# Performance work log

Hardware: AMD Instinct MI355X
Metric: run time of the kernel (lower is better)

Reference implementation:

```python
import jax, jax.numpy as jnp
from jax import lax
import numpy as np

H = 512      # hidden_size
NF = 64      # nfeatures
NL = 2       # num_layers
OUT = 1      # output_size
B, T = 64, 512


def _uniform(key, shape, scale):
    return jax.random.uniform(key, shape, jnp.float32, -scale, scale)


def setup_inputs() -> dict:
    key = jax.random.key(0)
    ks = jax.random.split(key, 12)
    s = 1.0 / np.sqrt(H)  # PyTorch LSTM/Linear init scale
    return {
        "x": jax.random.normal(ks[0], (B, T, NF), jnp.float32),
        # layer 0 (input NF -> H), PyTorch gate order i,f,g,o along 4H axis
        "W_ih0": _uniform(ks[1], (4 * H, NF), s),
        "W_hh0": _uniform(ks[2], (4 * H, H), s),
        "b_ih0": _uniform(ks[3], (4 * H,), s),
        "b_hh0": _uniform(ks[4], (4 * H,), s),
        # layer 1 (input H -> H)
        "W_ih1": _uniform(ks[5], (4 * H, H), s),
        "W_hh1": _uniform(ks[6], (4 * H, H), s),
        "b_ih1": _uniform(ks[7], (4 * H,), s),
        "b_hh1": _uniform(ks[8], (4 * H,), s),
        # final linear head
        "W_fc": _uniform(ks[9], (OUT, H), s),
        "b_fc": _uniform(ks[10], (OUT,), s),
    }


def _lstm_layer(x, W_ih, W_hh, b_ih, b_hh):
    """x: [B, T, D_in] -> hidden sequence [B, T, H]. Zero initial state."""
    b, t, _ = x.shape
    h0 = jnp.zeros((b, H), x.dtype)
    c0 = jnp.zeros((b, H), x.dtype)
    # precompute input projections for all timesteps: [T, B, 4H]
    xp = jnp.swapaxes(jnp.einsum('btd,gd->btg', x, W_ih) + b_ih + b_hh, 0, 1)

    def step(carry, xt):
        h, c = carry
        gates = xt + h @ W_hh.T  # [B, 4H]
        i, f, g, o = jnp.split(gates, 4, axis=-1)
        i = jax.nn.sigmoid(i)
        f = jax.nn.sigmoid(f)
        g = jnp.tanh(g)
        o = jax.nn.sigmoid(o)
        c = f * c + i * g
        h = o * jnp.tanh(c)
        return (h, c), h

    _, hs = lax.scan(step, (h0, c0), xp)  # hs: [T, B, H]
    return jnp.swapaxes(hs, 0, 1)


def reference(x, W_ih0, W_hh0, b_ih0, b_hh0, W_ih1, W_hh1, b_ih1, b_hh1, W_fc, b_fc):
    h = _lstm_layer(x, W_ih0, W_hh0, b_ih0, b_hh0)
    h = _lstm_layer(h, W_ih1, W_hh1, b_ih1, b_hh1)
    return h @ W_fc.T + b_fc  # [B, T, OUT]
```

## Files before the change

kernel.cpp:

```cpp
#include <hip/hip_runtime.h>

#define T_STEPS 512
#define BATCH   64
#define HID     512

typedef __attribute__((ext_vector_type(8))) short short8;
typedef __attribute__((ext_vector_type(4))) float f32x4;

__device__ __forceinline__ unsigned short f2bf(float f){
  unsigned u = __float_as_uint(f);
  u += 0x7FFF + ((u >> 16) & 1);
  return (unsigned short)(u >> 16);
}
__device__ __forceinline__ float bf2f(unsigned short s){
  return __uint_as_float(((unsigned)s) << 16);
}
__device__ __forceinline__ f32x4 mfma16(short8 a, short8 b, f32x4 c){
  return __builtin_amdgcn_mfma_f32_16x16x32_bf16(a, b, c, 0, 0, 0);
}
__device__ __forceinline__ float sigf(float x){
  return 1.0f / (1.0f + exp2f(-1.44269504f * x));
}
__device__ __forceinline__ float tanh_(float x){
  float e = exp2f(2.88539008f * x);
  return 1.0f - 2.0f / (1.0f + e);
}


__device__ __forceinline__ void pollL0(const int* flags0, int target){
  if (threadIdx.x < 64){
    int lane = threadIdx.x;
    int guard = 0;
    for (;;){
      int v = (lane < 32)
        ? __hip_atomic_load(&flags0[lane*32], __ATOMIC_RELAXED, __HIP_MEMORY_SCOPE_AGENT)
        : target;
      if (__ballot(v >= target) == ~0ull) break;
      __builtin_amdgcn_s_sleep(1);
      if (++guard > (1 << 20)) break;
    }
  }
  __builtin_amdgcn_fence(__ATOMIC_ACQUIRE, "workgroup");
  asm volatile("" ::: "memory");
  __syncthreads();
}

__device__ __forceinline__ void pollL1(const int* flags0, const int* flags1, int t){
  if (threadIdx.x < 64){
    int lane = threadIdx.x;
    const int* p = (lane < 32) ? &flags0[lane*32] : &flags1[(lane-32)*32];
    int tgt = (lane < 32) ? t + 1 : t;
    int guard = 0;
    for (;;){
      int v = __hip_atomic_load(p, __ATOMIC_RELAXED, __HIP_MEMORY_SCOPE_AGENT);
      if (__ballot(v >= tgt) == ~0ull) break;
      __builtin_amdgcn_s_sleep(1);
      if (++guard > (1 << 20)) break;
    }
  }
  __builtin_amdgcn_fence(__ATOMIC_ACQUIRE, "workgroup");
  asm volatile("" ::: "memory");
  __syncthreads();
}

__device__ __forceinline__ void signalSlot(int* slot, int val){
  __builtin_amdgcn_fence(__ATOMIC_RELEASE, "workgroup");
  asm volatile("" ::: "memory");
  __hip_atomic_store(slot, val, __ATOMIC_RELAXED, __HIP_MEMORY_SCOPE_AGENT);
}

template<int NKB>
__device__ __forceinline__ void loadB(const unsigned short* __restrict__ Wg, int K, int kstart,
                                      int l15, int l4, short8 B[4][NKB]){
  #pragma unroll
  for (int tt = 0; tt < 4; ++tt)
    #pragma unroll
    for (int kb = 0; kb < NKB; ++kb)
      B[tt][kb] = *(const short8*)(Wg + (long)(tt*16 + l15)*K + kstart + kb*32 + l4*8);
}

template<int NKB>
__device__ __forceinline__ void gemmA(const unsigned short* __restrict__ Ab, long rs,
                                      int l15, int l4, const short8 B[4][NKB], f32x4 acc[4][4]){
  #pragma unroll
  for (int kb = 0; kb < NKB; ++kb){
    short8 a[4];
    #pragma unroll
    for (int m = 0; m < 4; ++m)
      a[m] = *(const short8*)(Ab + (long)(m*16 + l15)*rs + kb*32 + l4*8);
    #pragma unroll
    for (int m = 0; m < 4; ++m)
      #pragma unroll
      for (int tt = 0; tt < 4; ++tt)
        acc[m][tt] = mfma16(B[tt][kb], a[m], acc[m][tt]);
  }
}

__device__ __forceinline__ void reduceWrite(float* red, int w, int l15, int l4, f32x4 acc[4][4]){
  #pragma unroll
  for (int m = 0; m < 4; ++m){
    if (m == w) continue;
    int mi = (m > w) ? m - 1 : m;
    #pragma unroll
    for (int tt = 0; tt < 4; ++tt){
      float* p = red + (w*12 + mi*4 + tt)*320 + l15*20 + l4*4;
      *(f32x4*)p = acc[m][tt];
    }
  }
}
__device__ __forceinline__ void reduceRead(const float* red, int w, int l15, int l4,
                                           f32x4 gf[4], f32x4 acc[4][4]){
  #pragma unroll
  for (int tt = 0; tt < 4; ++tt) gf[tt] = acc[w][tt];
  #pragma unroll
  for (int v = 0; v < 4; ++v){
    if (v == w) continue;
    int mi = (w > v) ? w - 1 : w;
    #pragma unroll
    for (int tt = 0; tt < 4; ++tt){
      const float* p = red + (v*12 + mi*4 + tt)*320 + l15*20 + l4*4;
      gf[tt] += *(const f32x4*)p;
    }
  }
}

__device__ __forceinline__ void gatesStore(f32x4 gf[4], f32x4& cst,
                                           unsigned short* __restrict__ hdst){
  f32x4 hh;
  #pragma unroll
  for (int r = 0; r < 4; ++r){
    float iv = sigf(gf[0][r]), fv = sigf(gf[1][r]);
    float gv = tanh_(gf[2][r]), ov = sigf(gf[3][r]);
    float cv = fv * cst[r] + iv * gv;
    cst[r] = cv;
    hh[r] = ov * tanh_(cv);
  }
  unsigned long long pk = (unsigned long long)f2bf(hh[0])
    | ((unsigned long long)f2bf(hh[1]) << 16)
    | ((unsigned long long)f2bf(hh[2]) << 32)
    | ((unsigned long long)f2bf(hh[3]) << 48);
  __hip_atomic_store((unsigned long long*)hdst, pk, __ATOMIC_RELAXED, __HIP_MEMORY_SCOPE_AGENT);
}

template<int NXB, int NHB>
__device__ void l0_loop(int g, int w, int lane,
                        const unsigned short* __restrict__ Wg,
                        const float* __restrict__ bias0,
                        const unsigned short* __restrict__ xb,
                        unsigned short* __restrict__ h0seq,
                        int* flags0, float* red, int hk0){
  int l15 = lane & 15, l4 = lane >> 4;
  short8 Bx[4][(NXB > 0) ? NXB : 1];
  if constexpr (NXB > 0) loadB<NXB>(Wg, 576, 0, l15, l4, Bx);
  short8 Bh[4][NHB];
  loadB<NHB>(Wg, 576, 64 + hk0, l15, l4, Bh);
  f32x4 bsv[4];
  #pragma unroll
  for (int tt = 0; tt < 4; ++tt) bsv[tt] = *(const f32x4*)&bias0[(g*4 + tt)*16 + l4*4];
  f32x4 cst = {0.f, 0.f, 0.f, 0.f};
  int b = w*16 + l15, colb = g*16 + l4*4;

  for (int t = 0; t < T_STEPS; ++t){
    f32x4 acc[4][4];
    #pragma unroll
    for (int m = 0; m < 4; ++m)
      #pragma unroll
      for (int tt = 0; tt < 4; ++tt) acc[m][tt] = (f32x4){0.f,0.f,0.f,0.f};
    if constexpr (NXB > 0)
      gemmA<NXB>(xb + (long)t*64, (long)T_STEPS*64, l15, l4, Bx, acc);
    if (t) pollL0(flags0, t);
    if (t)
      gemmA<NHB>(h0seq + (long)(t-1)*BATCH*HID + hk0, HID, l15, l4, Bh, acc);
    reduceWrite(red, w, l15, l4, acc);
    __syncthreads();
    f32x4 gf[4];
    reduceRead(red, w, l15, l4, gf, acc);
    #pragma unroll
    for (int tt = 0; tt < 4; ++tt) gf[tt] += bsv[tt];
    gatesStore(gf, cst, h0seq + (long)t*BATCH*HID + (long)b*HID + colb);
    __syncthreads();
    if (threadIdx.x == 0) signalSlot(&flags0[g*32], t + 1);
  }
}

__device__ void l1_loop(int g, int w, int lane,
                        const unsigned short* __restrict__ Wg,
                        const float* __restrict__ bias1,
                        const unsigned short* __restrict__ h0seq,
                        unsigned short* __restrict__ h1seq,
                        int* flags0, int* flags1, float* red){
  int l15 = lane & 15, l4 = lane >> 4;
  short8 Bh[4][8];
  loadB<8>(Wg, 1024, w*256, l15, l4, Bh);
  f32x4 bsv[4];
  #pragma unroll
  for (int tt = 0; tt < 4; ++tt) bsv[tt] = *(const f32x4*)&bias1[(g*4 + tt)*16 + l4*4];
  f32x4 cst = {0.f, 0.f, 0.f, 0.f};
  int b = w*16 + l15, colb = g*16 + l4*4;

  for (int t = 0; t < T_STEPS; ++t){
    pollL1(flags0, flags1, t);
    f32x4 acc[4][4];
    #pragma unroll
    for (int m = 0; m < 4; ++m)
      #pragma unroll
      for (int tt = 0; tt < 4; ++tt) acc[m][tt] = (f32x4){0.f,0.f,0.f,0.f};
    if (w < 2)
      gemmA<8>(h0seq + (long)t*BATCH*HID + w*256, HID, l15, l4, Bh, acc);
    else if (t)
      gemmA<8>(h1seq + (long)(t-1)*BATCH*HID + (w-2)*256, HID, l15, l4, Bh, acc);
    reduceWrite(red, w, l15, l4, acc);
    __syncthreads();
    f32x4 gf[4];
    reduceRead(red, w, l15, l4, gf, acc);
    #pragma unroll
    for (int tt = 0; tt < 4; ++tt) gf[tt] += bsv[tt];
    gatesStore(gf, cst, h1seq + (long)t*BATCH*HID + (long)b*HID + colb);
    __syncthreads();
    if (threadIdx.x == 0) signalSlot(&flags1[g*32], t + 1);
  }
}

extern "C" __global__ void __launch_bounds__(256, 1)
lstm_persist(const unsigned short* __restrict__ Wpk0,
             const unsigned short* __restrict__ Wpk1,
             const float* __restrict__ bias0, const float* __restrict__ bias1,
             const unsigned short* __restrict__ xb,
             unsigned short* __restrict__ h0seq, unsigned short* __restrict__ h1seq,
             int* flags0, int* flags1){
  __shared__ float red[15360];
  int wg = blockIdx.x;
  int role = wg >> 5;
  int g = wg & 31;
  int w = threadIdx.x >> 6;
  int lane = threadIdx.x & 63;

  if (role == 0){
    const unsigned short* Wg = Wpk0 + (long)g*4*16*576;
    switch (w){
      case 0:  l0_loop<2,3>(g, 0, lane, Wg, bias0, xb, h0seq, flags0, red, 0);   break;
      case 1:  l0_loop<0,5>(g, 1, lane, Wg, bias0, xb, h0seq, flags0, red, 96);  break;
      case 2:  l0_loop<0,4>(g, 2, lane, Wg, bias0, xb, h0seq, flags0, red, 256); break;
      default: l0_loop<0,4>(g, 3, lane, Wg, bias0, xb, h0seq, flags0, red, 384); break;
    }
  } else {
    const unsigned short* Wg = Wpk1 + (long)g*4*16*1024;
    l1_loop(g, w, lane, Wg, bias1, h0seq, h1seq, flags0, flags1, red);
  }
}

extern "C" __global__ void prep_kernel(const float* __restrict__ x,
    const float* __restrict__ Wih0, const float* __restrict__ Whh0,
    const float* __restrict__ bih0, const float* __restrict__ bhh0,
    const float* __restrict__ Wih1, const float* __restrict__ Whh1,
    const float* __restrict__ bih1, const float* __restrict__ bhh1,
    unsigned short* __restrict__ Wpk0, unsigned short* __restrict__ Wpk1,
    float* __restrict__ bias0, float* __restrict__ bias1,
    unsigned short* __restrict__ xb, int* __restrict__ syncm){
  long gid = (long)blockIdx.x * blockDim.x + threadIdx.x;
  long gs  = (long)gridDim.x * blockDim.x;
  const long NW0 = 32L*4*16*576;
  const long NW1 = 32L*4*16*1024;
  const long NX  = 64L*512*64;

  for (long i = gid; i < NW0; i += gs){
    int k = (int)(i % 576);
    long q = i / 576;
    int r  = (int)(q & 15);
    long q2 = q >> 4;
    int tt = (int)(q2 & 3);
    int g  = (int)(q2 >> 2);
    int row = tt*512 + g*16 + r;
    float v = (k < 64) ? Wih0[(long)row*64 + k] : Whh0[(long)row*512 + (k - 64)];
    Wpk0[i] = f2bf(v);
  }
  for (long i = gid; i < NW1; i += gs){
    int k = (int)(i & 1023);
    long q = i >> 10;
    int r  = (int)(q & 15);
    long q2 = q >> 4;
    int tt = (int)(q2 & 3);
    int g  = (int)(q2 >> 2);
    int row = tt*512 + g*16 + r;
    float v = (k < 512) ? Wih1[(long)row*512 + k] : Whh1[(long)row*512 + (k - 512)];
    Wpk1[i] = f2bf(v);
  }
  for (long i = gid; i < 2048; i += gs){
    int r = (int)(i & 15);
    int tt = (int)((i >> 4) & 3);
    int g  = (int)(i >> 6);
    int row = tt*512 + g*16 + r;
    bias0[i] = bih0[row] + bhh0[row];
    bias1[i] = bih1[row] + bhh1[row];
  }
  for (long i = gid; i < NX; i += gs) xb[i] = f2bf(x[i]);
  for (long i = gid; i < 2048; i += gs) syncm[i] = 0;
}

extern "C" __global__ void head_kernel(const unsigned short* __restrict__ h1seq,
    const float* __restrict__ wfc, const float* __restrict__ bfc,
    float* __restrict__ out){
  int t = blockIdx.x;
  int tid = threadIdx.x;
  int b = tid >> 2, q = tid & 3;
  const unsigned short* hp = h1seq + ((long)t*BATCH + b)*HID + q*128;
  const float* wp = wfc + q*128;
  float s = 0.f;
  #pragma unroll
  for (int i = 0; i < 16; ++i){
    short8 v = *(const short8*)(hp + i*8);
    #pragma unroll
    for (int e = 0; e < 8; ++e)
      s += bf2f((unsigned short)v[e]) * wp[i*8 + e];
  }
  s += __shfl_xor(s, 1, 64);
  s += __shfl_xor(s, 2, 64);
  if (q == 0) out[(long)b*T_STEPS + t] = s + bfc[0];
}

extern "C" void kernel_launch(void* const* d_in, const int* in_sizes, int n_in,
                              void* d_out, int out_size, void* d_ws, size_t ws_size,
                              hipStream_t stream){
  const float* x    = (const float*)d_in[0];
  const float* Wih0 = (const float*)d_in[1];
  const float* Whh0 = (const float*)d_in[2];
  const float* bih0 = (const float*)d_in[3];
  const float* bhh0 = (const float*)d_in[4];
  const float* Wih1 = (const float*)d_in[5];
  const float* Whh1 = (const float*)d_in[6];
  const float* bih1 = (const float*)d_in[7];
  const float* bhh1 = (const float*)d_in[8];
  const float* wfc  = (const float*)d_in[9];
  const float* bfc  = (const float*)d_in[10];
  float* out = (float*)d_out;

  char* p = (char*)d_ws;
  auto carve = [&](size_t bytes) -> void* {
    void* r = (void*)p;
    p += (bytes + 255) & ~(size_t)255;
    return r;
  };
  unsigned short* Wpk0  = (unsigned short*)carve(32L*4*16*576*2);
  unsigned short* Wpk1  = (unsigned short*)carve(32L*4*16*1024*2);
  float* bias0 = (float*)carve(2048*4);
  float* bias1 = (float*)carve(2048*4);
  unsigned short* xb    = (unsigned short*)carve(64L*512*64*2);
  unsigned short* h0seq = (unsigned short*)carve(512L*64*512*2);
  unsigned short* h1seq = (unsigned short*)carve(512L*64*512*2);
  int* syncm   = (int*)carve(8192);
  int* flags0 = syncm;
  int* flags1 = syncm + 1024;

  hipLaunchKernelGGL(prep_kernel, dim3(1024), dim3(256), 0, stream,
                     x, Wih0, Whh0, bih0, bhh0, Wih1, Whh1, bih1, bhh1,
                     Wpk0, Wpk1, bias0, bias1, xb, syncm);
  hipLaunchKernelGGL(lstm_persist, dim3(64), dim3(256), 0, stream,
                     Wpk0, Wpk1, bias0, bias1, xb, h0seq, h1seq, flags0, flags1);
  hipLaunchKernelGGL(head_kernel, dim3(512), dim3(256), 0, stream,
                     h1seq, wfc, bfc, out);
}
```

Measured before the change: 5.261 ms.

## Co-locate persistent LSTM blocks on one XCD and use L2-scoped flag sync

Launches 512 blocks but keeps only every eighth one, so that under round-robin dispatch all 64 working blocks land on the same XCD. At startup the blocks check whether they can all see each other's flags through L2-coherent (sc0) loads. If they agree, they use sc0 loads and stores for the step flags and plain stores for the h outputs, instead of agent-scope atomics, and the spin loops drop `s_sleep`. The goal is lower cross-block handoff latency on each of the 512 serial timesteps. The cost is that the working blocks share fewer CUs, and correctness depends on the dispatch placement and on the verdict check; there is a fallback to the original atomic path.

Result: slower. 8.966 ms (+70.4%).

```diff
diff --git a/kernel.cpp b/kernel.cpp
--- a/kernel.cpp
+++ b/kernel.cpp
@@ -26,47 +26,56 @@
   return 1.0f - 2.0f / (1.0f + e);
 }
 
-
-__device__ __forceinline__ void pollL0(const int* flags0, int target){
-  if (threadIdx.x < 64){
-    int lane = threadIdx.x;
-    int guard = 0;
-    for (;;){
-      int v = (lane < 32)
-        ? __hip_atomic_load(&flags0[lane*32], __ATOMIC_RELAXED, __HIP_MEMORY_SCOPE_AGENT)
-        : target;
-      if (__ballot(v >= target) == ~0ull) break;
-      __builtin_amdgcn_s_sleep(1);
-      if (++guard > (1 << 20)) break;
-    }
-  }
+__device__ __forceinline__ int fload(const int* p){
+  int v;
+  asm volatile("global_load_dword %0, %1, off sc0\n\ts_waitcnt vmcnt(0)"
+               : "=&v"(v) : "v"(p) : "memory");
+  return v;
+}
+__device__ __forceinline__ void fstore(int* p, int v){
+  asm volatile("global_store_dword %0, %1, off sc0" :: "v"(p), "v"(v) : "memory");
+}
+__device__ __forceinline__ int aload(const int* p){
+  return __hip_atomic_load(p, __ATOMIC_RELAXED, __HIP_MEMORY_SCOPE_AGENT);
+}
+__device__ __forceinline__ void astore(int* p, int v){
+  __hip_atomic_store(p, v, __ATOMIC_RELAXED, __HIP_MEMORY_SCOPE_AGENT);
+}
+
+template<bool FAST>
+__device__ __forceinline__ void spin0(int* fF, int* fS, int target){
+  int lane = threadIdx.x & 63;
+  int idx = (lane & 31)*32;
+  int guard = 0;
+  for (;;){
+    int v = FAST ? fload(fF + idx) : aload(fS + idx);
+    if (__ballot(v >= target) == ~0ull) break;
+    if (++guard > (1 << 16)) break;
+  }
+  asm volatile("" ::: "memory");
   __builtin_amdgcn_fence(__ATOMIC_ACQUIRE, "workgroup");
+}
+template<bool FAST>
+__device__ __forceinline__ void spin1(int* f0F, int* f0S, int* f1F, int* f1S, int t){
+  int lane = threadIdx.x & 63;
+  int idx = (lane & 31)*32;
+  int tgt = (lane < 32) ? t + 1 : t;
+  int* pF = (lane < 32) ? f0F + idx : f1F + idx;
+  int* pS = (lane < 32) ? f0S + idx : f1S + idx;
+  int guard = 0;
+  for (;;){
+    int v = FAST ? fload(pF) : aload(pS);
+    if (__ballot(v >= tgt) == ~0ull) break;
+    if (++guard > (1 << 16)) break;
+  }
   asm volatile("" ::: "memory");
-  __syncthreads();
-}
-
-__device__ __forceinline__ void pollL1(const int* flags0, const int* flags1, int t){
-  if (threadIdx.x < 64){
-    int lane = threadIdx.x;
-    const int* p = (lane < 32) ? &flags0[lane*32] : &flags1[(lane-32)*32];
-    int tgt = (lane < 32) ? t + 1 : t;
-    int guard = 0;
-    for (;;){
-      int v = __hip_atomic_load(p, __ATOMIC_RELAXED, __HIP_MEMORY_SCOPE_AGENT);
-      if (__ballot(v >= tgt) == ~0ull) break;
-      __builtin_amdgcn_s_sleep(1);
-      if (++guard > (1 << 20)) break;
-    }
-  }
   __builtin_amdgcn_fence(__ATOMIC_ACQUIRE, "workgroup");
-  asm volatile("" ::: "memory");
-  __syncthreads();
-}
-
-__device__ __forceinline__ void signalSlot(int* slot, int val){
+}
+template<bool FAST>
+__device__ __forceinline__ void signal(int* slotF, int* slotS, int val){
   __builtin_amdgcn_fence(__ATOMIC_RELEASE, "workgroup");
   asm volatile("" ::: "memory");
-  __hip_atomic_store(slot, val, __ATOMIC_RELAXED, __HIP_MEMORY_SCOPE_AGENT);
+  if (FAST) fstore(slotF, val); else astore(slotS, val);
 }
 
 template<int NKB>
@@ -124,6 +133,7 @@
   }
 }
 
+template<bool FAST>
 __device__ __forceinline__ void gatesStore(f32x4 gf[4], f32x4& cst,
                                            unsigned short* __restrict__ hdst){
   f32x4 hh;
@@ -139,16 +149,19 @@
     | ((unsigned long long)f2bf(hh[1]) << 16)
     | ((unsigned long long)f2bf(hh[2]) << 32)
     | ((unsigned long long)f2bf(hh[3]) << 48);
-  __hip_atomic_store((unsigned long long*)hdst, pk, __ATOMIC_RELAXED, __HIP_MEMORY_SCOPE_AGENT);
-}
-
-template<int NXB, int NHB>
+  if (FAST)
+    *(unsigned long long*)hdst = pk;
+  else
+    __hip_atomic_store((unsigned long long*)hdst, pk, __ATOMIC_RELAXED, __HIP_MEMORY_SCOPE_AGENT);
+}
+
+template<int NXB, int NHB, bool FAST>
 __device__ void l0_loop(int g, int w, int lane,
                         const unsigned short* __restrict__ Wg,
                         const float* __restrict__ bias0,
                         const unsigned short* __restrict__ xb,
                         unsigned short* __restrict__ h0seq,
-                        int* flags0, float* red, int hk0){
+                        int* fF0, int* fS0, float* red, int hk0){
   int l15 = lane & 15, l4 = lane >> 4;
   short8 Bx[4][(NXB > 0) ? NXB : 1];
   if constexpr (NXB > 0) loadB<NXB>(Wg, 576, 0, l15, l4, Bx);
@@ -168,27 +181,29 @@
       for (int tt = 0; tt < 4; ++tt) acc[m][tt] = (f32x4){0.f,0.f,0.f,0.f};
     if constexpr (NXB > 0)
       gemmA<NXB>(xb + (long)t*64, (long)T_STEPS*64, l15, l4, Bx, acc);
-    if (t) pollL0(flags0, t);
-    if (t)
+    if (t){
+      spin0<FAST>(fF0, fS0, t);
       gemmA<NHB>(h0seq + (long)(t-1)*BATCH*HID + hk0, HID, l15, l4, Bh, acc);
+    }
     reduceWrite(red, w, l15, l4, acc);
     __syncthreads();
     f32x4 gf[4];
     reduceRead(red, w, l15, l4, gf, acc);
     #pragma unroll
     for (int tt = 0; tt < 4; ++tt) gf[tt] += bsv[tt];
-    gatesStore(gf, cst, h0seq + (long)t*BATCH*HID + (long)b*HID + colb);
+    gatesStore<FAST>(gf, cst, h0seq + (long)t*BATCH*HID + (long)b*HID + colb);
     __syncthreads();
-    if (threadIdx.x == 0) signalSlot(&flags0[g*32], t + 1);
-  }
-}
-
+    if (threadIdx.x == 0) signal<FAST>(&fF0[g*32], &fS0[g*32], t + 1);
+  }
+}
+
+template<bool FAST>
 __device__ void l1_loop(int g, int w, int lane,
                         const unsigned short* __restrict__ Wg,
                         const float* __restrict__ bias1,
                         const unsigned short* __restrict__ h0seq,
                         unsigned short* __restrict__ h1seq,
-                        int* flags0, int* flags1, float* red){
+                        int* fF0, int* fS0, int* fF1, int* fS1, float* red){
   int l15 = lane & 15, l4 = lane >> 4;
   short8 Bh[4][8];
   loadB<8>(Wg, 1024, w*256, l15, l4, Bh);
@@ -199,7 +214,7 @@
   int b = w*16 + l15, colb = g*16 + l4*4;
 
   for (int t = 0; t < T_STEPS; ++t){
-    pollL1(flags0, flags1, t);
+    spin1<FAST>(fF0, fS0, fF1, fS1, t);
     f32x4 acc[4][4];
     #pragma unroll
     for (int m = 0; m < 4; ++m)
@@ -215,37 +230,70 @@
     reduceRead(red, w, l15, l4, gf, acc);
     #pragma unroll
     for (int tt = 0; tt < 4; ++tt) gf[tt] += bsv[tt];
-    gatesStore(gf, cst, h1seq + (long)t*BATCH*HID + (long)b*HID + colb);
+    gatesStore<FAST>(gf, cst, h1seq + (long)t*BATCH*HID + (long)b*HID + colb);
     __syncthreads();
-    if (threadIdx.x == 0) signalSlot(&flags1[g*32], t + 1);
-  }
-}
-
-extern "C" __global__ void __launch_bounds__(256, 1)
+    if (threadIdx.x == 0) signal<FAST>(&fF1[g*32], &fS1[g*32], t + 1);
+  }
+}
+
+extern "C" __global__ void __launch_bounds__(256, 2)
 lstm_persist(const unsigned short* __restrict__ Wpk0,
              const unsigned short* __restrict__ Wpk1,
              const float* __restrict__ bias0, const float* __restrict__ bias1,
              const unsigned short* __restrict__ xb,
              unsigned short* __restrict__ h0seq, unsigned short* __restrict__ h1seq,
-             int* flags0, int* flags1){
+             int* fF0, int* fS0, int* fF1, int* fS1, int* xsig, int* verdict){
+  if (blockIdx.x & 7) return;
+  int slot = blockIdx.x >> 3;
   __shared__ float red[15360];
-  int wg = blockIdx.x;
-  int role = wg >> 5;
-  int g = wg & 31;
+  __shared__ int s_fast;
+
+  if (threadIdx.x == 0) fstore(&xsig[slot*32], 1);
+  if (threadIdx.x < 64){
+    int lane = threadIdx.x;
+    int seen = 0;
+    for (int it = 0; it < 512 && !seen; ++it){
+      int v = fload(&xsig[lane*32]);
+      if (__ballot(v != 0) == ~0ull) seen = 1;
+    }
+    if (threadIdx.x == 0) astore(&verdict[slot*32], seen ? 2 : 1);
+    int allfast = 0, guard = 0;
+    for (;;){
+      int v = aload(&verdict[lane*32]);
+      if (__ballot(v != 0) == ~0ull){ allfast = (__ballot(v == 2) == ~0ull); break; }
+      if (++guard > (1 << 19)) { allfast = 0; break; }
+    }
+    if (threadIdx.x == 0) s_fast = allfast;
+  }
+  __syncthreads();
+  bool FAST = (s_fast != 0);
+
+  int role = slot >> 5;
+  int g = slot & 31;
   int w = threadIdx.x >> 6;
   int lane = threadIdx.x & 63;
 
   if (role == 0){
     const unsigned short* Wg = Wpk0 + (long)g*4*16*576;
-    switch (w){
-      case 0:  l0_loop<2,3>(g, 0, lane, Wg, bias0, xb, h0seq, flags0, red, 0);   break;
-      case 1:  l0_loop<0,5>(g, 1, lane, Wg, bias0, xb, h0seq, flags0, red, 96);  break;
-      case 2:  l0_loop<0,4>(g, 2, lane, Wg, bias0, xb, h0seq, flags0, red, 256); break;
-      default: l0_loop<0,4>(g, 3, lane, Wg, bias0, xb, h0seq, flags0, red, 384); break;
+    if (FAST){
+      switch (w){
+        case 0:  l0_loop<2,3,true>(g, 0, lane, Wg, bias0, xb, h0seq, fF0, fS0, red, 0);   break;
+        case 1:  l0_loop<0,5,true>(g, 1, lane, Wg, bias0, xb, h0seq, fF0, fS0, red, 96);  break;
+        case 2:  l0_loop<0,4,true>(g, 2, lane, Wg, bias0, xb, h0seq, fF0, fS0, red, 256); break;
+        default: l0_loop<0,4,true>(g, 3, lane, Wg, bias0, xb, h0seq, fF0, fS0, red, 384); break;
+      }
+    } else {
+      switch (w){
+        case 0:  l0_loop<2,3,false>(g, 0, lane, Wg, bias0, xb, h0seq, fF0, fS0, red, 0);   break;
+        case 1:  l0_loop<0,5,false>(g, 1, lane, Wg, bias0, xb, h0seq, fF0, fS0, red, 96);  break;
+        case 2:  l0_loop<0,4,false>(g, 2, lane, Wg, bias0, xb, h0seq, fF0, fS0, red, 256); break;
+        default: l0_loop<0,4,false>(g, 3, lane, Wg, bias0, xb, h0seq, fF0, fS0, red, 384); break;
+      }
     }
   } else {
     const unsigned short* Wg = Wpk1 + (long)g*4*16*1024;
-    l1_loop(g, w, lane, Wg, bias1, h0seq, h1seq, flags0, flags1, red);
+    if (FAST) l1_loop<true >(g, w, lane, Wg, bias1, h0seq, h1seq, fF0, fS0, fF1, fS1, red);
+    else      l1_loop<false>(g, w, lane, Wg, bias1, h0seq, h1seq, fF0, fS0, fF1, fS1, red);
   }
 }
 
@@ -294,7 +342,7 @@
     bias1[i] = bih1[row] + bhh1[row];
   }
   for (long i = gid; i < NX; i += gs) xb[i] = f2bf(x[i]);
-  for (long i = gid; i < 2048; i += gs) syncm[i] = 0;
+  for (long i = gid; i < 8192; i += gs) syncm[i] = 0;
 }
 
 extern "C" __global__ void head_kernel(const unsigned short* __restrict__ h1seq,
@@ -347,15 +395,20 @@
   unsigned short* xb    = (unsigned short*)carve(64L*512*64*2);
   unsigned short* h0seq = (unsigned short*)carve(512L*64*512*2);
   unsigned short* h1seq = (unsigned short*)carve(512L*64*512*2);
-  int* syncm   = (int*)carve(8192);
-  int* flags0 = syncm;
-  int* flags1 = syncm + 1024;
+  int* syncm   = (int*)carve(32768);
+  int* fF0     = syncm;
+  int* fS0     = syncm + 1024;
+  int* fF1     = syncm + 2048;
+  int* fS1     = syncm + 3072;
+  int* xsig    = syncm + 4096;
+  int* verdict = syncm + 6144;
 
   hipLaunchKernelGGL(prep_kernel, dim3(1024), dim3(256), 0, stream,
                      x, Wih0, Whh0, bih0, bhh0, Wih1, Whh1, bih1, bhh1,
                      Wpk0, Wpk1, bias0, bias1, xb, syncm);
-  hipLaunchKernelGGL(lstm_persist, dim3(64), dim3(256), 0, stream,
-                     Wpk0, Wpk1, bias0, bias1, xb, h0seq, h1seq, flags0, flags1);
+  hipLaunchKernelGGL(lstm_persist, dim3(512), dim3(256), 0, stream,
+                     Wpk0, Wpk1, bias0, bias1, xb, h0seq, h1seq,
+                     fF0, fS0, fF1, fS1, xsig, verdict);
   hipLaunchKernelGGL(head_kernel, dim3(512), dim3(256), 0, stream,
                      h1seq, wfc, bfc, out);
 }
```
